# Kernel tuning notes

Hardware: AMD Instinct MI355X
Metric: run time of the kernel (lower is better)

Reference implementation:

```python
import jax, jax.numpy as jnp
import numpy as np

KH, KW, STRIDE, PAD = 3, 3, 1, 1


def unfold(img, kh, kw, stride, padding):
    # torch.nn.functional.unfold, transposed to [B, L, C*kh*kw] with (c, kh, kw)-major ordering
    b, c, h, w = img.shape
    p = jnp.pad(img, ((0, 0), (0, 0), (padding, padding), (padding, padding)))
    oh = (h - kh + 2 * padding) // stride + 1
    ow = (w - kw + 2 * padding) // stride + 1
    # [b, c, kh*kw, oh, ow]; static python loop over the 9 kernel offsets only
    cols = jnp.stack([p[:, :, i:i + oh * stride:stride, j:j + ow * stride:stride]
                      for i in range(kh) for j in range(kw)], axis=2)
    return cols.reshape(b, c * kh * kw, oh * ow).transpose(0, 2, 1), oh, ow


def setup_inputs() -> dict:
    key = jax.random.key(0)
    k1, k2 = jax.random.split(key)
    img = jax.random.normal(k1, (8, 64, 112, 112), dtype=jnp.float32)
    weights = 0.8 * jax.random.normal(k2, (64, 64, 3, 3), dtype=jnp.float32)
    return {"img": img, "weights": weights}


def reference(img, weights):
    b = img.shape[0]
    O = weights.shape[0]
    W = weights.reshape(O, -1)            # [O, K], K = in_ch*kh*kw
    K = W.shape[1]
    u, oh, ow = unfold(img, KH, KW, STRIDE, PAD)   # [b, L, K]
    u2 = u * u
    u3 = u2 * u

    def gemm(poly):
        return jnp.einsum('blk,ok->blo', poly, W)

    # f: identity-kernel term has all-zero coefficients (p00=p10=p20=p30=0) -> drops out
    f = gemm(-0.000287 + 0.266 * u - 0.1097 * u2) / 75

    # identity_kernel is all ones, so (const*ones) @ ones.T == const * K (scalar)
    g1 = (0.11 / 75) * K + gemm(0.001309 + 0.00619 * u - 0.009 * u2 + 0.001383 * u3)
    g2 = (0.179 / 75) * K + gemm(-0.0025 + 0.00303 * u - 0.00484 * u2 + 0.0175 * u3)
    g3 = (0.238 / 75) * K + gemm(-0.000954 + 0.00187 * u + 0.001877 * u2 + 0.01502 * u3)
    g4 = (0.388 / 75) * K + gemm(-0.00734 + 0.001117 * u + 0.00752 * u2 + 0.009 * u3)
    g5 = (0.507 / 75) * K + gemm(-0.01017 + 0.000426 * u + 0.00837 * u2 + 0.00413 * u3)

    sig = jax.nn.sigmoid
    s1 = sig(10 * (0.15 - f))
    s2 = sig(10 * (f - 0.15)) + sig(10 * (0.23 - f)) - 1
    s3 = sig(10 * (f - 0.23)) + sig(10 * (0.32 - f)) - 1
    s4 = sig(10 * (f - 0.32)) + sig(10 * (0.39 - f)) - 1
    s5 = sig(10 * (f - 0.39))

    out = s1 * g1 + s2 * g2 + s3 * g3 + s4 * g4 + s5 * g5   # [b, L, O]
    return out.transpose(0, 2, 1).reshape(b, O, oh, ow)
```

## Files before the change

kernel.cpp:

```cpp
#include <hip/hip_runtime.h>

#define HW   112
#define KK   576

typedef __attribute__((ext_vector_type(8))) short s16x8;
typedef __attribute__((ext_vector_type(4))) float f32x4;
typedef __attribute__((ext_vector_type(2))) float f32x2;

#define LP_ROW   1184
#define LP_PHASE (10 * LP_ROW)
#define SWZ(px)  (((px) & 3) ^ (((px) >> 2) & 3))

__device__ inline unsigned short f2bf(float f) {
    unsigned u = __float_as_uint(f);
    u += 0x7FFF + ((u >> 16) & 1);
    return (unsigned short)(u >> 16);
}
__device__ inline unsigned pack2(float lo, float hi) {
    unsigned r;
    asm("v_cvt_pk_bf16_f32 %0, %1, %2" : "=v"(r) : "v"(lo), "v"(hi));
    return r;
}

__global__ __launch_bounds__(256) void prep_w(const float* __restrict__ W,
                                              unsigned short* __restrict__ wb,
                                              float* __restrict__ S) {
    const int bid = blockIdx.x, t = threadIdx.x;
    if (bid < 144) {
        const int i   = bid * 256 + t;
        const int j   = i & 7;
        const int l   = (i >> 3) & 63;
        const int nt  = (i >> 9) & 3;
        const int cc  = (i >> 11) & 1;
        const int tap = i >> 12;
        const int c   = cc * 32 + ((l >> 4) << 3) + j;
        const int o   = nt * 16 + (l & 15);
        wb[i] = f2bf(W[o * KK + c * 9 + tap]);
    } else {
        __shared__ float partial[256];
        const int o = t >> 2, part = t & 3;
        const float4* row = (const float4*)(W + o * KK) + part * 36;
        float s = 0.f;
        for (int k = 0; k < 36; ++k) { float4 v = row[k]; s += v.x + v.y + v.z + v.w; }
        partial[t] = s;
        __syncthreads();
        if (part == 0) S[o] = partial[t] + partial[t + 1] + partial[t + 2] + partial[t + 3];
    }
}

__global__ __launch_bounds__(256, 2) void conv_fused(const float* __restrict__ img,
                                                     const unsigned short* __restrict__ wb,
                                                     const float* __restrict__ S,
                                                     float* __restrict__ out) {
    __shared__ __align__(16) char tile[2][3 * LP_PHASE];

    const int t = threadIdx.x, wv = t >> 6, lane = t & 63;
    const int m = lane & 15, q = lane >> 4;

    const int bid = blockIdx.x;
    const int b = bid & 7;
    const int rest = bid >> 3;
    const int oc2 = rest & 1;
    const int r = rest >> 1;
    const int ty = r / 7, tx = r - ty * 7;
    const int y0 = ty * 8, x0 = tx * 16;

    f32x4 acc[3][2][2];
    #pragma unroll
    for (int p = 0; p < 3; ++p)
        #pragma unroll
        for (int at = 0; at < 2; ++at)
            #pragma unroll
            for (int ntl = 0; ntl < 2; ++ntl)
                acc[p][at][ntl] = (f32x4){0.f, 0.f, 0.f, 0.f};

    const char* wbase = (const char*)wb + oc2 * 2048 + lane * 16;
    s16x8 bfr[9][2];

    const int cp = t & 15, srow = t >> 4;
    const int sy = y0 + srow - 1;

    auto loadW = [&](int cc) {
        #pragma unroll
        for (int tap = 0; tap < 9; ++tap)
            #pragma unroll
            for (int ntl = 0; ntl < 2; ++ntl)
                bfr[tap][ntl] = *(const s16x8*)(wbase + (tap * 2 + cc) * 4096 + ntl * 1024);
    };

    auto load_va = [&](int cc, float (&va)[2][18]) {
        if (t >= 160) return;
        if (sy < 0 || sy >= HW) {
            #pragma unroll
            for (int e = 0; e < 2; ++e)
                #pragma unroll
                for (int px = 0; px < 18; ++px) va[e][px] = 0.f;
        } else {
            #pragma unroll
            for (int e = 0; e < 2; ++e) {
                const float* rp = img + ((size_t)(b * 64 + cc * 32 + cp * 2 + e) * HW + sy) * HW;
                va[e][0] = (x0 > 0) ? rp[x0 - 1] : 0.f;
                #pragma unroll
                for (int i2 = 0; i2 < 4; ++i2) {
                    const float4 v = *(const float4*)(rp + x0 + i2 * 4);
                    va[e][1 + 4 * i2] = v.x;
                    va[e][2 + 4 * i2] = v.y;
                    va[e][3 + 4 * i2] = v.z;
                    va[e][4 + 4 * i2] = v.w;
                }
                va[e][17] = (x0 + 16 < HW) ? rp[x0 + 16] : 0.f;
            }
        }
    };

    auto pack_write = [&](const float (&va)[2][18], char* buf) {
        if (t >= 160) return;
        char* wp = buf + srow * LP_ROW + (cp & 3) * 4;
        #pragma unroll
        for (int px = 0; px < 18; ++px) {
            char* a0 = wp + px * 64 + (((cp >> 2) ^ SWZ(px)) << 4);
            const float l1 = va[0][px], h1 = va[1][px];
            const float l2 = l1 * l1,   h2 = h1 * h1;
            const float l3 = l2 * l1,   h3 = h2 * h1;
            *(unsigned*)(a0)                = pack2(l1, h1);
            *(unsigned*)(a0 + LP_PHASE)     = pack2(l2, h2);
            *(unsigned*)(a0 + 2 * LP_PHASE) = pack2(l3, h3);
        }
    };

    auto compute_plane = [&](const char* bufbase, int p) {
        const char* base = bufbase + p * LP_PHASE;
        #pragma unroll
        for (int kx = 0; kx < 3; ++kx) {
            const int pxr  = m + kx;
            const int c8sr = q ^ SWZ(pxr);
            const int abase = wv * (2 * LP_ROW) + pxr * 64 + c8sr * 16;
            s16x8 af[4];
            #pragma unroll
            for (int r4 = 0; r4 < 4; ++r4)
                af[r4] = *(const s16x8*)&base[abase + r4 * LP_ROW];
            __builtin_amdgcn_s_setprio(1);
            #pragma unroll
            for (int ky = 0; ky < 3; ++ky)
                #pragma unroll
                for (int at = 0; at < 2; ++at)
                    #pragma unroll
                    for (int ntl = 0; ntl < 2; ++ntl)
                        acc[p][at][ntl] = __builtin_amdgcn_mfma_f32_16x16x32_bf16(
                            af[at + ky], bfr[ky * 3 + kx][ntl], acc[p][at][ntl], 0, 0, 0);
            __builtin_amdgcn_s_setprio(0);
        }
    };

    {
        float va[2][18];
        load_va(0, va);
        pack_write(va, tile[0]);
    }
    loadW(0);
    __syncthreads();

    {
        float vb[2][18];
        load_va(1, vb);
        compute_plane(tile[0], 0);
        pack_write(vb, tile[1]);
    }
    compute_plane(tile[0], 1);
    compute_plane(tile[0], 2);
    loadW(1);
    __syncthreads();

    compute_plane(tile[1], 0);
    compute_plane(tile[1], 1);
    compute_plane(tile[1], 2);

    #pragma unroll
    for (int ntl = 0; ntl < 2; ++ntl) {
        const int o = (oc2 * 2 + ntl) * 16 + (lane & 15);
        const float Sv = S[o];
        const float fS = -0.000287f / 75.f * Sv;
        const float cg1 = 0.8448f  + 0.001309f * Sv;
        const float D1  = 0.52992f - 0.003809f * Sv;
        const float D2  = 0.45312f + 0.001546f * Sv;
        const float D3  = 1.152f   - 0.006386f * Sv;
        const float D4  = 0.91392f - 0.00283f  * Sv;
        #pragma unroll
        for (int at = 0; at < 2; ++at) {
            float res[4];
            #pragma unroll
            for (int h = 0; h < 2; ++h) {
                const f32x2 u1 = {acc[0][at][ntl][2 * h], acc[0][at][ntl][2 * h + 1]};
                const f32x2 u2 = {acc[1][at][ntl][2 * h], acc[1][at][ntl][2 * h + 1]};
                const f32x2 u3 = {acc[2][at][ntl][2 * h], acc[2][at][ntl][2 * h + 1]};
                const f32x2 f  = fS   + 0.00354667f * u1 - 0.00146267f * u2;
                const f32x2 g1 = cg1  + 0.00619f    * u1 - 0.009f      * u2 + 0.001383f * u3;
                const f32x2 d1 = D1   - 0.00316f    * u1 + 0.00416f    * u2 + 0.016117f * u3;
                const f32x2 d2 = D2   - 0.00116f    * u1 + 0.006717f   * u2 - 0.00248f  * u3;
                const f32x2 d3 = D3   - 0.000753f   * u1 + 0.005643f   * u2 - 0.00602f  * u3;
                const f32x2 d4 = D4   - 0.000691f   * u1 + 0.00085f    * u2 - 0.00487f  * u3;
                f32x2 E;
                E.x = __expf(-10.f * f.x);
                E.y = __expf(-10.f * f.y);
                const f32x2 den1 = 1.f + E * 4.4816890703f;
                const f32x2 den2 = 1.f + E * 9.9741824548f;
                const f32x2 den3 = 1.f + E * 24.5325301971f;
                const f32x2 den4 = 1.f + E * 49.4024491055f;
                f32x2 o2 = g1;
                o2.x += __builtin_amdgcn_rcpf(den1.x) * d1.x + __builtin_amdgcn_rcpf(den2.x) * d2.x
                      + __builtin_amdgcn_rcpf(den3.x) * d3.x + __builtin_amdgcn_rcpf(den4.x) * d4.x;
                o2.y += __builtin_amdgcn_rcpf(den1.y) * d1.y + __builtin_amdgcn_rcpf(den2.y) * d2.y
                      + __builtin_amdgcn_rcpf(den3.y) * d3.y + __builtin_amdgcn_rcpf(den4.y) * d4.y;
                res[2 * h] = o2.x; res[2 * h + 1] = o2.y;
            }
            const int y = y0 + 2 * wv + at;
            float* op = out + (((size_t)(b * 64 + o)) * HW + y) * HW + x0 + q * 4;
            *(float4*)op = make_float4(res[0], res[1], res[2], res[3]);
        }
    }
}

extern "C" void kernel_launch(void* const* d_in, const int* in_sizes, int n_in,
                              void* d_out, int out_size, void* d_ws, size_t ws_size,
                              hipStream_t stream) {
    const float* img = (const float*)d_in[0];
    const float* w   = (const float*)d_in[1];
    float* outp = (float*)d_out;
    unsigned short* wb = (unsigned short*)d_ws;
    float* S = (float*)(wb + 36864);

    hipLaunchKernelGGL(prep_w,     dim3(145),  dim3(256), 0, stream, w, wb, S);
    hipLaunchKernelGGL(conv_fused, dim3(1568), dim3(256), 0, stream, img, wb, S, outp);
}
```

Baseline: 110.3 us.

## Merge output-channel halves into one 512-thread block sharing the input tile

Each block now has 8 waves, and the two groups of four waves compute the two 32-channel output halves. This replaces two separate blocks that each staged the same input tile. Both channel chunks are loaded and packed into shared memory at once by 320 threads, followed by a single barrier. The aim is to halve the redundant global loads and the poly/pack work per tile. The cost is losing the overlap of the second chunk's load with compute, plus a larger block with launch bounds of 512 threads and 4 blocks per CU, which may pressure registers.

```diff
diff --git a/kernel.cpp b/kernel.cpp
--- a/kernel.cpp
+++ b/kernel.cpp
@@ -48,20 +48,19 @@
     }
 }
 
-__global__ __launch_bounds__(256, 2) void conv_fused(const float* __restrict__ img,
+__global__ __launch_bounds__(512, 4) void conv_fused(const float* __restrict__ img,
                                                      const unsigned short* __restrict__ wb,
                                                      const float* __restrict__ S,
                                                      float* __restrict__ out) {
     __shared__ __align__(16) char tile[2][3 * LP_PHASE];
 
     const int t = threadIdx.x, wv = t >> 6, lane = t & 63;
+    const int wvr = wv & 3, oc2 = wv >> 2;
     const int m = lane & 15, q = lane >> 4;
 
     const int bid = blockIdx.x;
     const int b = bid & 7;
-    const int rest = bid >> 3;
-    const int oc2 = rest & 1;
-    const int r = rest >> 1;
+    const int r = bid >> 3;
     const int ty = r / 7, tx = r - ty * 7;
     const int y0 = ty * 8, x0 = tx * 16;
 
@@ -77,9 +76,6 @@
     const char* wbase = (const char*)wb + oc2 * 2048 + lane * 16;
     s16x8 bfr[9][2];
 
-    const int cp = t & 15, srow = t >> 4;
-    const int sy = y0 + srow - 1;
-
     auto loadW = [&](int cc) {
         #pragma unroll
         for (int tap = 0; tap < 9; ++tap)
@@ -88,45 +84,49 @@
                 bfr[tap][ntl] = *(const s16x8*)(wbase + (tap * 2 + cc) * 4096 + ntl * 1024);
     };
 
-    auto load_va = [&](int cc, float (&va)[2][18]) {
-        if (t >= 160) return;
-        if (sy < 0 || sy >= HW) {
-            #pragma unroll
-            for (int e = 0; e < 2; ++e)
+    {
+        const int scc  = (t >= 160) ? 1 : 0;
+        const int su   = t - scc * 160;
+        const int cp   = su & 15, srow = su >> 4;
+        const int sy   = y0 + srow - 1;
+        if (t < 320) {
+            float va[2][18];
+            if (sy < 0 || sy >= HW) {
                 #pragma unroll
-                for (int px = 0; px < 18; ++px) va[e][px] = 0.f;
-        } else {
-            #pragma unroll
-            for (int e = 0; e < 2; ++e) {
-                const float* rp = img + ((size_t)(b * 64 + cc * 32 + cp * 2 + e) * HW + sy) * HW;
-                va[e][0] = (x0 > 0) ? rp[x0 - 1] : 0.f;
+                for (int e = 0; e < 2; ++e)
+                    #pragma unroll
+                    for (int px = 0; px < 18; ++px) va[e][px] = 0.f;
+            } else {
                 #pragma unroll
-                for (int i2 = 0; i2 < 4; ++i2) {
-                    const float4 v = *(const float4*)(rp + x0 + i2 * 4);
-                    va[e][1 + 4 * i2] = v.x;
-                    va[e][2 + 4 * i2] = v.y;
-                    va[e][3 + 4 * i2] = v.z;
-                    va[e][4 + 4 * i2] = v.w;
+                for (int e = 0; e < 2; ++e) {
+                    const float* rp = img + ((size_t)(b * 64 + scc * 32 + cp * 2 + e) * HW + sy) * HW;
+                    va[e][0] = (x0 > 0) ? rp[x0 - 1] : 0.f;
+                    #pragma unroll
+                    for (int i2 = 0; i2 < 4; ++i2) {
+                        const float4 v = *(const float4*)(rp + x0 + i2 * 4);
+                        va[e][1 + 4 * i2] = v.x;
+                        va[e][2 + 4 * i2] = v.y;
+                        va[e][3 + 4 * i2] = v.z;
+                        va[e][4 + 4 * i2] = v.w;
+                    }
+                    va[e][17] = (x0 + 16 < HW) ? rp[x0 + 16] : 0.f;
                 }
-                va[e][17] = (x0 + 16 < HW) ? rp[x0 + 16] : 0.f;
+            }
+            char* wp = tile[scc] + srow * LP_ROW + (cp & 3) * 4;
+            #pragma unroll
+            for (int px = 0; px < 18; ++px) {
+                char* a0 = wp + px * 64 + (((cp >> 2) ^ SWZ(px)) << 4);
+                const float l1 = va[0][px], h1 = va[1][px];
+                const float l2 = l1 * l1,   h2 = h1 * h1;
+                const float l3 = l2 * l1,   h3 = h2 * h1;
+                *(unsigned*)(a0)                = pack2(l1, h1);
+                *(unsigned*)(a0 + LP_PHASE)     = pack2(l2, h2);
+                *(unsigned*)(a0 + 2 * LP_PHASE) = pack2(l3, h3);
             }
         }
-    };
-
-    auto pack_write = [&](const float (&va)[2][18], char* buf) {
-        if (t >= 160) return;
-        char* wp = buf + srow * LP_ROW + (cp & 3) * 4;
-        #pragma unroll
-        for (int px = 0; px < 18; ++px) {
-            char* a0 = wp + px * 64 + (((cp >> 2) ^ SWZ(px)) << 4);
-            const float l1 = va[0][px], h1 = va[1][px];
-            const float l2 = l1 * l1,   h2 = h1 * h1;
-            const float l3 = l2 * l1,   h3 = h2 * h1;
-            *(unsigned*)(a0)                = pack2(l1, h1);
-            *(unsigned*)(a0 + LP_PHASE)     = pack2(l2, h2);
-            *(unsigned*)(a0 + 2 * LP_PHASE) = pack2(l3, h3);
-        }
-    };
+    }
+    loadW(0);
+    __syncthreads();
 
     auto compute_plane = [&](const char* bufbase, int p) {
         const char* base = bufbase + p * LP_PHASE;
@@ -134,7 +134,7 @@
         for (int kx = 0; kx < 3; ++kx) {
             const int pxr  = m + kx;
             const int c8sr = q ^ SWZ(pxr);
-            const int abase = wv * (2 * LP_ROW) + pxr * 64 + c8sr * 16;
+            const int abase = wvr * (2 * LP_ROW) + pxr * 64 + c8sr * 16;
             s16x8 af[4];
             #pragma unroll
             for (int r4 = 0; r4 < 4; ++r4)
@@ -152,25 +152,10 @@
         }
     };
 
-    {
-        float va[2][18];
-        load_va(0, va);
-        pack_write(va, tile[0]);
-    }
-    loadW(0);
-    __syncthreads();
-
-    {
-        float vb[2][18];
-        load_va(1, vb);
-        compute_plane(tile[0], 0);
-        pack_write(vb, tile[1]);
-    }
+    compute_plane(tile[0], 0);
     compute_plane(tile[0], 1);
     compute_plane(tile[0], 2);
     loadW(1);
-    __syncthreads();
-
     compute_plane(tile[1], 0);
     compute_plane(tile[1], 1);
     compute_plane(tile[1], 2);
@@ -213,7 +198,7 @@
                       + __builtin_amdgcn_rcpf(den3.y) * d3.y + __builtin_amdgcn_rcpf(den4.y) * d4.y;
                 res[2 * h] = o2.x; res[2 * h + 1] = o2.y;
             }
-            const int y = y0 + 2 * wv + at;
+            const int y = y0 + 2 * wvr + at;
             float* op = out + (((size_t)(b * 64 + o)) * HW + y) * HW + x0 + q * 4;
             *(float4*)op = make_float4(res[0], res[1], res[2], res[3]);
         }
@@ -229,6 +214,6 @@
     unsigned short* wb = (unsigned short*)d_ws;
     float* S = (float*)(wb + 36864);
 
-    hipLaunchKernelGGL(prep_w,     dim3(145),  dim3(256), 0, stream, w, wb, S);
-    hipLaunchKernelGGL(conv_fused, dim3(1568), dim3(256), 0, stream, img, wb, S, outp);
-}
+    hipLaunchKernelGGL(prep_w,     dim3(145), dim3(256), 0, stream, w, wb, S);
+    hipLaunchKernelGGL(conv_fused, dim3(784), dim3(512), 0, stream, img, wb, S, outp);
+}
```

Result: slower. 125.5 us (+13.7%).
